# Optimization experiments

Hardware: AMD Instinct MI355X
Metric: run time of the kernel (lower is better)

## Reference

```python
import jax, jax.numpy as jnp
import numpy as np

B, T, D = 2, 2048, 1024
P, ALPHA, P_R = 512, 4, 64
HID = 16 * D
EPS = 1e-6


def rmsnorm(x, w):
    norm = jnp.sqrt(jnp.mean(x * x, axis=-1, keepdims=True) + EPS)
    return x * w / norm


def ssm_lowrank(t, F, b_r, c_r):
    # gated elementwise recurrence h_t = F_t * h_{t-1} + t_t, then low-rank correction
    Fs = jnp.moveaxis(F, 1, 0)   # (T,B,P)
    ts = jnp.moveaxis(t, 1, 0)   # (T,B,P)

    def step(h, inp):
        f, u = inp
        h = f * h + u
        return h, h

    h0 = jnp.zeros((t.shape[0], t.shape[2]), dtype=t.dtype)
    _, hs = jax.lax.scan(step, h0, (Fs, ts))
    h = jnp.moveaxis(hs, 0, 1)   # (B,T,P)
    t_tilde = t + jnp.einsum('btp,pr,rq->btq', h, b_r, c_r)
    return t_tilde


def setup_inputs() -> dict:
    key = jax.random.key(0)
    ks = jax.random.split(key, 11)
    s = lambda fan: 1.0 / np.sqrt(fan)
    return {
        'x':       jax.random.normal(ks[0], (B, T, D), jnp.float32),
        'w_norm1': jnp.ones((D,), jnp.float32),
        'w_toP':   jax.random.normal(ks[1], (D, P), jnp.float32) * s(D),
        'w_emb':   jax.random.normal(ks[2], (D, ALPHA * P), jnp.float32) * s(D),
        'w_f':     jax.random.normal(ks[3], (D, P), jnp.float32) * s(D),
        'b_r':     jax.random.normal(ks[4], (P, P_R), jnp.float32) * s(P),
        'c_r':     jax.random.normal(ks[5], (P_R, P), jnp.float32) * s(P_R),
        'w_fromP': jax.random.normal(ks[6], (P, D), jnp.float32) * s(P),
        'w_norm2': jnp.ones((D,), jnp.float32),
        'w_fc1':   jax.random.normal(ks[7], (D, HID), jnp.float32) * s(D),
        'w_fc2':   jax.random.normal(ks[8], (HID, D), jnp.float32) * s(HID),
    }


def reference(x, w_norm1, w_toP, w_emb, w_f, b_r, c_r, w_fromP, w_norm2, w_fc1, w_fc2):
    # ---- pre-LN CEPTA context path ----
    h1 = rmsnorm(x, w_norm1)
    pre_path = jnp.einsum('btd,dp->btp', h1, w_toP)                 # to_P
    U = jnp.einsum('btd,dk->btk', h1, w_emb).reshape(B, T, ALPHA, P)  # cepta_dense U
    Fgate = jax.nn.sigmoid(jnp.einsum('btd,dp->btp', h1, w_f))      # cepta_dense F
    Y = jax.nn.gelu(U)                                              # cepta_dense Y
    t = jnp.sum(Y, axis=2) + pre_path                               # router reduce='sum'
    t_tilde = ssm_lowrank(t, Fgate, b_r, c_r)                       # low-rank SSM
    y = jnp.einsum('btp,pd->btd', t_tilde, w_fromP)                 # from_P
    x = x + y
    # ---- pre-LN GELU MLP ----
    h2 = rmsnorm(x, w_norm2)
    z = jnp.einsum('bth,hd->btd', jax.nn.gelu(jnp.einsum('btd,dh->bth', h2, w_fc1)), w_fc2)
    return x + z
```

## Files before the change

kernel.cpp:

```cpp
#include <hip/hip_runtime.h>

typedef unsigned short u16;
typedef __bf16 bf16x8 __attribute__((ext_vector_type(8)));
typedef float f32x4 __attribute__((ext_vector_type(4)));
typedef int i32x4 __attribute__((ext_vector_type(4)));

__device__ inline u16 f2bf(float f) {
  union { float f; unsigned u; } v; v.f = f;
  unsigned u = v.u;
  unsigned r = (u + 0x7FFFu + ((u >> 16) & 1u)) >> 16;
  return (u16)r;
}

__device__ inline float gelu_f(float x) {
  float t = 0.7978845608028654f * (x + 0.044715f * x * x * x);
  float a = __expf(-2.f * fabsf(t));
  float th = (1.f - a) / (1.f + a);
  th = copysignf(th, t);
  return 0.5f * x * (1.f + th);
}
__device__ inline float sigmoid_f(float x) { return 1.f / (1.f + __expf(-x)); }

__device__ __forceinline__ void gld16(const u16* g, u16* l) {
  __builtin_amdgcn_global_load_lds((const __attribute__((address_space(1))) void*)g,
                                   (__attribute__((address_space(3))) void*)l, 16, 0, 0);
}
__device__ __forceinline__ bf16x8 ld_frag(const u16* p) {
  return __builtin_bit_cast(bf16x8, *(const i32x4*)p);
}

__global__ void transpose_cvt(const float* __restrict__ in, u16* __restrict__ out,
                              int R, int C, int ldout) {
  __shared__ float tile[32][33];
  int c0 = blockIdx.x * 32, r0 = blockIdx.y * 32;
  int tx = threadIdx.x, ty = threadIdx.y;
#pragma unroll
  for (int i = 0; i < 32; i += 8) {
    int r = r0 + ty + i, c = c0 + tx;
    tile[ty + i][tx] = (r < R && c < C) ? in[(long)r * C + c] : 0.f;
  }
  __syncthreads();
#pragma unroll
  for (int i = 0; i < 32; i += 8) {
    int cc = c0 + ty + i, rr = r0 + tx;
    if (cc < C && rr < R) out[(long)cc * ldout + rr] = f2bf(tile[tx][ty + i]);
  }
}

__global__ __launch_bounds__(256) void rmsnorm_k(const float* __restrict__ x,
                                                 const float* __restrict__ w,
                                                 u16* __restrict__ out) {
  int row = blockIdx.x;
  int tid = threadIdx.x;
  const float4* xv = (const float4*)(x + (long)row * 1024);
  float4 v = xv[tid];
  float ss = v.x * v.x + v.y * v.y + v.z * v.z + v.w * v.w;
#pragma unroll
  for (int off = 32; off > 0; off >>= 1) ss += __shfl_down(ss, off);
  __shared__ float red[4];
  if ((tid & 63) == 0) red[tid >> 6] = ss;
  __syncthreads();
  float tot = red[0] + red[1] + red[2] + red[3];
  float scale = rsqrtf(tot * (1.f / 1024.f) + 1e-6f);
  const float4* wv4 = (const float4*)w;
  float4 wv = wv4[tid];
  ushort4 o;
  o.x = f2bf(v.x * wv.x * scale);
  o.y = f2bf(v.y * wv.y * scale);
  o.z = f2bf(v.z * wv.z * scale);
  o.w = f2bf(v.w * wv.w * scale);
  *((ushort4*)(out + (long)row * 1024) + tid) = o;
}

#define EPI_BF16 0
#define EPI_ROUTE1 1
#define EPI_ADD_BF16 2
#define EPI_ADD_F32 3
#define EPI_GELU_BF16 4
#define EPI_PART 5

template <int EPI>
__global__ __launch_bounds__(512, 2) void gemm256(
    const u16* __restrict__ A, const u16* __restrict__ Bt,
    u16* __restrict__ obf, float* __restrict__ of32,
    float* __restrict__ og, float* __restrict__ ofl,
    int N, int K, int lda, int ldb) {
  __shared__ __align__(16) u16 sA[2][16384];
  __shared__ __align__(16) u16 sB[2][16384];
  const int tid = threadIdx.x;
  const int lane = tid & 63;
  const int wave = tid >> 6;
  const int wm = wave >> 2, wn = wave & 3;
  const int lane15 = lane & 15;

  const int gx = gridDim.x, gy = gridDim.y, gz = gridDim.z;
  const int nwg = gx * gy * gz;
  int orig = (blockIdx.z * gy + blockIdx.y) * gx + blockIdx.x;
  int id = ((nwg & 7) == 0) ? ((orig & 7) * (nwg >> 3) + (orig >> 3)) : orig;
  const int bx = id % gx;
  const int by = (id / gx) % gy;
  const int bz = id / (gx * gy);
  const int bm0 = by * 256, bn0 = bx * 256;
  const int kper = K / gz, koff = bz * kper;

  f32x4 acc[8][4];
  f32x4 zero = {0.f, 0.f, 0.f, 0.f};
#pragma unroll
  for (int m = 0; m < 8; ++m)
#pragma unroll
    for (int n = 0; n < 4; ++n) acc[m][n] = zero;

  const int grow = tid >> 2;
  const int gck = ((tid & 3) ^ ((tid >> 3) & 3)) << 3;
  const u16* ag = A + (long)(bm0 + grow) * lda + koff + gck;
  const u16* bg = Bt + (long)(bn0 + grow) * ldb + koff + gck;
  const long a128 = (long)128 * lda, b128 = (long)128 * ldb;
  const int wofs = wave << 9;

  const int coff = (((lane >> 4) ^ ((lane15 >> 1) & 3)) << 3);
  const int rbrow = (wn & 1) * 64 + lane15;
  const int bsegh = (wn >> 1) * 2;

  const int nk = kper >> 6;

  gld16(ag, &sA[0][0 * 4096 + wofs]);
  gld16(ag + a128, &sA[0][2 * 4096 + wofs]);
  gld16(bg, &sB[0][0 * 4096 + wofs]);
  gld16(bg + b128, &sB[0][2 * 4096 + wofs]);
  gld16(ag + 32, &sA[0][1 * 4096 + wofs]);
  gld16(ag + a128 + 32, &sA[0][3 * 4096 + wofs]);
  gld16(bg + 32, &sB[0][1 * 4096 + wofs]);
  gld16(bg + b128 + 32, &sB[0][3 * 4096 + wofs]);

  bf16x8 av[4], bv[4];
#define DSRD_B(kk)                                                                   \
  _Pragma("unroll") for (int n = 0; n < 4; ++n)                                      \
      bv[n] = ld_frag(rB + (bsegh + kk) * 4096 + (rbrow + n * 16) * 32 + coff);
#define DSRD_A(kk, mh)                                                               \
  _Pragma("unroll") for (int m = 0; m < 4; ++m)                                      \
      av[m] = ld_frag(rA + (wm * 2 + kk) * 4096 + (mh * 64 + m * 16 + lane15) * 32 + coff);
#define MFMA16(mh)                                                                   \
  __builtin_amdgcn_s_setprio(1);                                                     \
  _Pragma("unroll") for (int m = 0; m < 4; ++m)                                      \
      _Pragma("unroll") for (int n = 0; n < 4; ++n)                                  \
          acc[mh * 4 + m][n] =                                                       \
              __builtin_amdgcn_mfma_f32_16x16x32_bf16(av[m], bv[n], acc[mh * 4 + m][n], 0, 0, 0); \
  __builtin_amdgcn_s_setprio(0);
#define WAIT4()                                     \
  asm volatile("s_waitcnt vmcnt(4)" ::: "memory");  \
  __builtin_amdgcn_s_barrier();                     \
  asm volatile("" ::: "memory")
#define WAIT0()                                     \
  asm volatile("s_waitcnt vmcnt(0)" ::: "memory");  \
  __builtin_amdgcn_s_barrier();                     \
  asm volatile("" ::: "memory")

  int p = 0;
  for (int t = 0; t < nk - 1; ++t) {
    const u16* agn = ag + (long)(t + 1) * 64;
    const u16* bgn = bg + (long)(t + 1) * 64;
    u16* dA = &sA[p ^ 1][0];
    u16* dB = &sB[p ^ 1][0];
    const u16* rA = &sA[p][0];
    const u16* rB = &sB[p][0];
    WAIT4();
    DSRD_B(0);
    DSRD_A(0, 0);
    gld16(agn, dA + 0 * 4096 + wofs);
    gld16(agn + a128, dA + 2 * 4096 + wofs);
    MFMA16(0);
    DSRD_A(0, 1);
    gld16(bgn, dB + 0 * 4096 + wofs);
    gld16(bgn + b128, dB + 2 * 4096 + wofs);
    MFMA16(1);
    WAIT4();
    DSRD_B(1);
    DSRD_A(1, 0);
    gld16(agn + 32, dA + 1 * 4096 + wofs);
    gld16(agn + a128 + 32, dA + 3 * 4096 + wofs);
    MFMA16(0);
    DSRD_A(1, 1);
    gld16(bgn + 32, dB + 1 * 4096 + wofs);
    gld16(bgn + b128 + 32, dB + 3 * 4096 + wofs);
    MFMA16(1);
    p ^= 1;
  }
  {
    const u16* rA = &sA[p][0];
    const u16* rB = &sB[p][0];
    WAIT4();
    DSRD_B(0);
    DSRD_A(0, 0);
    MFMA16(0);
    DSRD_A(0, 1);
    MFMA16(1);
    WAIT0();
    DSRD_B(1);
    DSRD_A(1, 0);
    MFMA16(0);
    DSRD_A(1, 1);
    MFMA16(1);
  }
#undef DSRD_B
#undef DSRD_A
#undef MFMA16
#undef WAIT4
#undef WAIT0

#pragma unroll
  for (int M = 0; M < 8; ++M) {
    int row_b = bm0 + wm * 128 + M * 16 + ((lane >> 4) << 2);
#pragma unroll
    for (int n = 0; n < 4; ++n) {
      int col = bn0 + wn * 64 + n * 16 + lane15;
#pragma unroll
      for (int j = 0; j < 4; ++j) {
        int row = row_b + j;
        float v = acc[M][n][j];
        if constexpr (EPI == EPI_GELU_BF16) {
          obf[(long)row * N + col] = f2bf(gelu_f(v));
        } else if constexpr (EPI == EPI_ROUTE1) {
          if (col < 512) of32[(long)row * 512 + col] = v;
          else if (col < 2560) og[(long)row * 2048 + (col - 512)] = gelu_f(v);
          else ofl[(long)row * 512 + (col - 2560)] = sigmoid_f(v);
        } else {
          of32[(long)bz * (4096L * 1024) + (long)row * N + col] = v;
        }
      }
    }
  }
}

template <int EPI>
__global__ __launch_bounds__(256) void gemm_bt(
    const u16* __restrict__ A, const u16* __restrict__ Bt,
    u16* __restrict__ obf, float* __restrict__ of32, const float* __restrict__ add,
    float* __restrict__ og, float* __restrict__ ofl,
    int N, int K, int lda, int ldb) {
  __shared__ __align__(16) u16 As[128 * 64];
  __shared__ __align__(16) u16 Bs[128 * 64];
  const int tid = threadIdx.x;
  const int lane = tid & 63;
  const int wave = tid >> 6;
  const int wm = wave >> 1, wn = wave & 1;
  const int bm0 = blockIdx.y * 128, bn0 = blockIdx.x * 128;

  f32x4 acc[4][4];
  f32x4 zero = {0.f, 0.f, 0.f, 0.f};
#pragma unroll
  for (int m = 0; m < 4; ++m)
#pragma unroll
    for (int n = 0; n < 4; ++n) acc[m][n] = zero;

  i32x4 ra[4], rb[4];
  int srow[4], schk[4];
#pragma unroll
  for (int i = 0; i < 4; ++i) {
    int s = tid + 256 * i;
    srow[i] = s >> 3;
    schk[i] = s & 7;
  }
#pragma unroll
  for (int i = 0; i < 4; ++i) {
    ra[i] = *(const i32x4*)(A + (bm0 + srow[i]) * lda + schk[i] * 8);
    rb[i] = *(const i32x4*)(Bt + (bn0 + srow[i]) * ldb + schk[i] * 8);
  }

  const int nk = K >> 6;
  for (int t = 0; t < nk; ++t) {
#pragma unroll
    for (int i = 0; i < 4; ++i) {
      *(i32x4*)&As[srow[i] * 64 + ((schk[i] ^ (srow[i] & 7)) << 3)] = ra[i];
      *(i32x4*)&Bs[srow[i] * 64 + ((schk[i] ^ (srow[i] & 7)) << 3)] = rb[i];
    }
    __syncthreads();
    if (t + 1 < nk) {
      int k0 = (t + 1) << 6;
#pragma unroll
      for (int i = 0; i < 4; ++i) {
        ra[i] = *(const i32x4*)(A + (bm0 + srow[i]) * lda + k0 + schk[i] * 8);
        rb[i] = *(const i32x4*)(Bt + (bn0 + srow[i]) * ldb + k0 + schk[i] * 8);
      }
    }
#pragma unroll
    for (int kk = 0; kk < 2; ++kk) {
      bf16x8 av[4], bv[4];
#pragma unroll
      for (int m = 0; m < 4; ++m) {
        int r = wm * 64 + m * 16 + (lane & 15);
        int c = kk * 4 + (lane >> 4);
        av[m] = __builtin_bit_cast(bf16x8, *(const i32x4*)&As[r * 64 + ((c ^ (r & 7)) << 3)]);
      }
#pragma unroll
      for (int n = 0; n < 4; ++n) {
        int r = wn * 64 + n * 16 + (lane & 15);
        int c = kk * 4 + (lane >> 4);
        bv[n] = __builtin_bit_cast(bf16x8, *(const i32x4*)&Bs[r * 64 + ((c ^ (r & 7)) << 3)]);
      }
#pragma unroll
      for (int m = 0; m < 4; ++m)
#pragma unroll
        for (int n = 0; n < 4; ++n)
          acc[m][n] = __builtin_amdgcn_mfma_f32_16x16x32_bf16(av[m], bv[n], acc[m][n], 0, 0, 0);
    }
    __syncthreads();
  }

#pragma unroll
  for (int m = 0; m < 4; ++m) {
    int row_b = bm0 + wm * 64 + m * 16 + ((lane >> 4) << 2);
#pragma unroll
    for (int n = 0; n < 4; ++n) {
      int col = bn0 + wn * 64 + n * 16 + (lane & 15);
#pragma unroll
      for (int j = 0; j < 4; ++j) {
        int row = row_b + j;
        float v = acc[m][n][j];
        if constexpr (EPI == EPI_BF16) {
          obf[(long)row * N + col] = f2bf(v);
        } else if constexpr (EPI == EPI_ADD_BF16) {
          long idx = (long)row * N + col;
          obf[idx] = f2bf(add[idx] + v);
        } else if constexpr (EPI == EPI_ADD_F32) {
          long idx = (long)row * N + col;
          of32[idx] = add[idx] + v;
        }
      }
    }
  }
}

__global__ __launch_bounds__(256) void reduce4_k(const float* __restrict__ base,
                                                 const float* __restrict__ p,
                                                 float* __restrict__ o) {
  long i = (long)blockIdx.x * 256 + threadIdx.x;
  const long PL = 4096L * 1024 / 4;
  float4 b = ((const float4*)base)[i];
  float4 q0 = ((const float4*)p)[i];
  float4 q1 = ((const float4*)p)[i + PL];
  float4 q2 = ((const float4*)p)[i + 2 * PL];
  float4 q3 = ((const float4*)p)[i + 3 * PL];
  float4 r;
  r.x = b.x + q0.x + q1.x + q2.x + q3.x;
  r.y = b.y + q0.y + q1.y + q2.y + q3.y;
  r.z = b.z + q0.z + q1.z + q2.z + q3.z;
  r.w = b.w + q0.w + q1.w + q2.w + q3.w;
  ((float4*)o)[i] = r;
}

__global__ __launch_bounds__(256) void router_k(float* __restrict__ tb, const float* __restrict__ G) {
  int i = blockIdx.x * 256 + threadIdx.x;
  int r = i >> 7, pq = i & 127;
  float4 t = ((float4*)tb)[i];
#pragma unroll
  for (int a = 0; a < 4; ++a) {
    float4 g = *((const float4*)(G + (long)r * 2048 + a * 512) + pq);
    t.x += g.x; t.y += g.y; t.z += g.z; t.w += g.w;
  }
  ((float4*)tb)[i] = t;
}

__global__ void scan_chunk(const float* __restrict__ tb, const float* __restrict__ F,
                           float* __restrict__ abuf, float* __restrict__ ubuf) {
  int b = blockIdx.x >> 5, c = blockIdx.x & 31, pidx = threadIdx.x;
  const float* fp = F + ((long)(b * 2048 + c * 64) * 512) + pidx;
  const float* up = tb + ((long)(b * 2048 + c * 64) * 512) + pidx;
  float A = 1.f, U = 0.f;
#pragma unroll 8
  for (int s = 0; s < 64; ++s) {
    float f = fp[(long)s * 512], u = up[(long)s * 512];
    A = f * A;
    U = f * U + u;
  }
  abuf[(b * 32 + c) * 512 + pidx] = A;
  ubuf[(b * 32 + c) * 512 + pidx] = U;
}

__global__ void scan_combine(const float* __restrict__ abuf, const float* __restrict__ ubuf,
                             float* __restrict__ hstart) {
  int b = blockIdx.x, pidx = threadIdx.x;
  float h = 0.f;
  for (int c = 0; c < 32; ++c) {
    hstart[(b * 32 + c) * 512 + pidx] = h;
    h = abuf[(b * 32 + c) * 512 + pidx] * h + ubuf[(b * 32 + c) * 512 + pidx];
  }
}

__global__ void scan_apply(const float* __restrict__ tb, const float* __restrict__ F,
                           const float* __restrict__ hstart, u16* __restrict__ hbf) {
  int b = blockIdx.x >> 5, c = blockIdx.x & 31, pidx = threadIdx.x;
  const float* fp = F + ((long)(b * 2048 + c * 64) * 512) + pidx;
  const float* up = tb + ((long)(b * 2048 + c * 64) * 512) + pidx;
  u16* op = hbf + ((long)(b * 2048 + c * 64) * 512) + pidx;
  float h = hstart[(b * 32 + c) * 512 + pidx];
#pragma unroll 8
  for (int s = 0; s < 64; ++s) {
    float f = fp[(long)s * 512], u = up[(long)s * 512];
    h = f * h + u;
    op[(long)s * 512] = f2bf(h);
  }
}

extern "C" void kernel_launch(void* const* d_in, const int* in_sizes, int n_in,
                              void* d_out, int out_size, void* d_ws, size_t ws_size,
                              hipStream_t stream) {
  const float* x       = (const float*)d_in[0];
  const float* w_norm1 = (const float*)d_in[1];
  const float* w_toP   = (const float*)d_in[2];
  const float* w_emb   = (const float*)d_in[3];
  const float* w_f     = (const float*)d_in[4];
  const float* b_r     = (const float*)d_in[5];
  const float* c_r     = (const float*)d_in[6];
  const float* w_fromP = (const float*)d_in[7];
  const float* w_norm2 = (const float*)d_in[8];
  const float* w_fc1   = (const float*)d_in[9];
  const float* w_fc2   = (const float*)d_in[10];
  float* out = (float*)d_out;

  char* base = (char*)d_ws;
  size_t off = 0;
  auto alloc = [&](size_t bytes) {
    void* r = base + off;
    off += (bytes + 255) & ~(size_t)255;
    return r;
  };
  u16* W1T     = (u16*)alloc((size_t)3072 * 1024 * 2);
  u16* WfromPT = (u16*)alloc((size_t)1024 * 512 * 2);
  u16* Wfc1T   = (u16*)alloc((size_t)16384 * 1024 * 2);
  u16* Wfc2T   = (u16*)alloc((size_t)1024 * 16384 * 2);
  u16* BrT     = (u16*)alloc((size_t)128 * 512 * 2);
  u16* CrT     = (u16*)alloc((size_t)512 * 128 * 2);
  u16* h1      = (u16*)alloc((size_t)4096 * 1024 * 2);
  float* G     = (float*)alloc((size_t)4096 * 2048 * 4);
  float* F     = (float*)alloc((size_t)4096 * 512 * 4);
  float* tb    = (float*)alloc((size_t)4096 * 512 * 4);
  float* abuf  = (float*)alloc((size_t)2 * 32 * 512 * 4);
  float* ubuf  = (float*)alloc((size_t)2 * 32 * 512 * 4);
  float* hstart= (float*)alloc((size_t)2 * 32 * 512 * 4);
  u16* hbf     = (u16*)alloc((size_t)4096 * 512 * 2);
  u16* g1buf   = (u16*)alloc((size_t)4096 * 128 * 2);
  u16* tt      = (u16*)alloc((size_t)4096 * 512 * 2);
  float* xmid  = (float*)alloc((size_t)4096 * 1024 * 4);
  u16* h2      = (u16*)alloc((size_t)4096 * 1024 * 2);
  u16* a3      = (u16*)alloc((size_t)4096 * 8192 * 2);
  float* part  = (float*)h1;
  (void)ws_size; (void)in_sizes; (void)n_in; (void)out_size;

  dim3 tpb(32, 8);
  transpose_cvt<<<dim3(16, 32), tpb, 0, stream>>>(w_toP, W1T, 1024, 512, 1024);
  transpose_cvt<<<dim3(64, 32), tpb, 0, stream>>>(w_emb, W1T + (size_t)512 * 1024, 1024, 2048, 1024);
  transpose_cvt<<<dim3(16, 32), tpb, 0, stream>>>(w_f, W1T + (size_t)2560 * 1024, 1024, 512, 1024);
  transpose_cvt<<<dim3(32, 16), tpb, 0, stream>>>(w_fromP, WfromPT, 512, 1024, 512);
  transpose_cvt<<<dim3(512, 32), tpb, 0, stream>>>(w_fc1, Wfc1T, 1024, 16384, 1024);
  transpose_cvt<<<dim3(32, 512), tpb, 0, stream>>>(w_fc2, Wfc2T, 16384, 1024, 16384);
  hipMemsetAsync(BrT, 0, (size_t)128 * 512 * 2, stream);
  hipMemsetAsync(CrT, 0, (size_t)512 * 128 * 2, stream);
  transpose_cvt<<<dim3(2, 16), tpb, 0, stream>>>(b_r, BrT, 512, 64, 512);
  transpose_cvt<<<dim3(16, 2), tpb, 0, stream>>>(c_r, CrT, 64, 512, 128);

  rmsnorm_k<<<4096, 256, 0, stream>>>(x, w_norm1, h1);

  gemm256<EPI_ROUTE1><<<dim3(12, 16, 1), 512, 0, stream>>>(h1, W1T, nullptr, tb, G, F,
                                                           3072, 1024, 1024, 1024);
  router_k<<<2048, 256, 0, stream>>>(tb, G);

  scan_chunk<<<64, 512, 0, stream>>>(tb, F, abuf, ubuf);
  scan_combine<<<2, 512, 0, stream>>>(abuf, ubuf, hstart);
  scan_apply<<<64, 512, 0, stream>>>(tb, F, hstart, hbf);

  gemm_bt<EPI_BF16><<<dim3(1, 32), 256, 0, stream>>>(hbf, BrT, g1buf, nullptr, nullptr, nullptr, nullptr,
                                                     128, 512, 512, 512);
  gemm_bt<EPI_ADD_BF16><<<dim3(4, 32), 256, 0, stream>>>(g1buf, CrT, tt, nullptr, tb, nullptr, nullptr,
                                                         512, 128, 128, 128);
  gemm_bt<EPI_ADD_F32><<<dim3(8, 32), 256, 0, stream>>>(tt, WfromPT, nullptr, xmid, x, nullptr, nullptr,
                                                        1024, 512, 512, 512);
  rmsnorm_k<<<4096, 256, 0, stream>>>(xmid, w_norm2, h2);

  for (int c = 0; c < 2; ++c) {
    gemm256<EPI_GELU_BF16><<<dim3(32, 16, 1), 512, 0, stream>>>(
        h2, Wfc1T + (size_t)c * 8192 * 1024, a3, nullptr, nullptr, nullptr,
        8192, 1024, 1024, 1024);
    gemm256<EPI_PART><<<dim3(4, 16, 4), 512, 0, stream>>>(
        a3, Wfc2T + (size_t)c * 8192, nullptr, part, nullptr, nullptr,
        1024, 8192, 8192, 16384);
    reduce4_k<<<4096, 256, 0, stream>>>((c == 0 ? xmid : out), part, out);
  }
}
```

Measured before the change: 537.6 us.

## Rewrite small GEMM with async LDS double-buffering and route first projection through it

Replaces the register-staged 128x128 GEMM with a double-buffered version that uses direct global-to-LDS loads, split-K half-tile waits, MFMA priority hints and a workgroup-index swizzle for cache locality. The first fused projection (to_P/emb/F) moves from the 256-tile kernel to this 128-tile kernel with a larger grid to raise occupancy. The low-rank and from_P GEMMs also use it. This adds more LDS per block and depends on the vmcnt-based wait counting being correct.

New measurement: 538.4 us. No clear change (+0.2%).

```diff
diff --git a/kernel.cpp b/kernel.cpp
--- a/kernel.cpp
+++ b/kernel.cpp
@@ -232,18 +232,26 @@
 }
 
 template <int EPI>
-__global__ __launch_bounds__(256) void gemm_bt(
+__global__ __launch_bounds__(256, 2) void gemm128(
     const u16* __restrict__ A, const u16* __restrict__ Bt,
     u16* __restrict__ obf, float* __restrict__ of32, const float* __restrict__ add,
     float* __restrict__ og, float* __restrict__ ofl,
     int N, int K, int lda, int ldb) {
-  __shared__ __align__(16) u16 As[128 * 64];
-  __shared__ __align__(16) u16 Bs[128 * 64];
+  __shared__ __align__(16) u16 sA[2][8192];
+  __shared__ __align__(16) u16 sB[2][8192];
   const int tid = threadIdx.x;
   const int lane = tid & 63;
   const int wave = tid >> 6;
   const int wm = wave >> 1, wn = wave & 1;
-  const int bm0 = blockIdx.y * 128, bn0 = blockIdx.x * 128;
+  const int lane15 = lane & 15;
+
+  const int gx = gridDim.x, gy = gridDim.y;
+  const int nwg = gx * gy;
+  int orig = blockIdx.y * gx + blockIdx.x;
+  int id = ((nwg & 7) == 0) ? ((orig & 7) * (nwg >> 3) + (orig >> 3)) : orig;
+  const int bx = id % gx;
+  const int by = id / gx;
+  const int bm0 = by * 128, bn0 = bx * 128;
 
   f32x4 acc[4][4];
   f32x4 zero = {0.f, 0.f, 0.f, 0.f};
@@ -252,70 +260,96 @@
 #pragma unroll
     for (int n = 0; n < 4; ++n) acc[m][n] = zero;
 
-  i32x4 ra[4], rb[4];
-  int srow[4], schk[4];
-#pragma unroll
-  for (int i = 0; i < 4; ++i) {
-    int s = tid + 256 * i;
-    srow[i] = s >> 3;
-    schk[i] = s & 7;
-  }
-#pragma unroll
-  for (int i = 0; i < 4; ++i) {
-    ra[i] = *(const i32x4*)(A + (bm0 + srow[i]) * lda + schk[i] * 8);
-    rb[i] = *(const i32x4*)(Bt + (bn0 + srow[i]) * ldb + schk[i] * 8);
-  }
+  const int grow = tid >> 2;
+  const int gck = ((tid & 3) ^ ((tid >> 3) & 3)) << 3;
+  const u16* ag = A + (long)(bm0 + grow) * lda + gck;
+  const u16* bg = Bt + (long)(bn0 + grow) * ldb + gck;
+  const long a64 = (long)64 * lda, b64 = (long)64 * ldb;
+  const int wofs = wave << 9;
+
+  const int coff = (((lane >> 4) ^ ((lane15 >> 1) & 3)) << 3);
 
   const int nk = K >> 6;
-  for (int t = 0; t < nk; ++t) {
-#pragma unroll
-    for (int i = 0; i < 4; ++i) {
-      *(i32x4*)&As[srow[i] * 64 + ((schk[i] ^ (srow[i] & 7)) << 3)] = ra[i];
-      *(i32x4*)&Bs[srow[i] * 64 + ((schk[i] ^ (srow[i] & 7)) << 3)] = rb[i];
-    }
-    __syncthreads();
-    if (t + 1 < nk) {
-      int k0 = (t + 1) << 6;
-#pragma unroll
-      for (int i = 0; i < 4; ++i) {
-        ra[i] = *(const i32x4*)(A + (bm0 + srow[i]) * lda + k0 + schk[i] * 8);
-        rb[i] = *(const i32x4*)(Bt + (bn0 + srow[i]) * ldb + k0 + schk[i] * 8);
-      }
-    }
-#pragma unroll
-    for (int kk = 0; kk < 2; ++kk) {
-      bf16x8 av[4], bv[4];
-#pragma unroll
-      for (int m = 0; m < 4; ++m) {
-        int r = wm * 64 + m * 16 + (lane & 15);
-        int c = kk * 4 + (lane >> 4);
-        av[m] = __builtin_bit_cast(bf16x8, *(const i32x4*)&As[r * 64 + ((c ^ (r & 7)) << 3)]);
-      }
-#pragma unroll
-      for (int n = 0; n < 4; ++n) {
-        int r = wn * 64 + n * 16 + (lane & 15);
-        int c = kk * 4 + (lane >> 4);
-        bv[n] = __builtin_bit_cast(bf16x8, *(const i32x4*)&Bs[r * 64 + ((c ^ (r & 7)) << 3)]);
-      }
-#pragma unroll
-      for (int m = 0; m < 4; ++m)
-#pragma unroll
-        for (int n = 0; n < 4; ++n)
-          acc[m][n] = __builtin_amdgcn_mfma_f32_16x16x32_bf16(av[m], bv[n], acc[m][n], 0, 0, 0);
-    }
-    __syncthreads();
-  }
-
-#pragma unroll
-  for (int m = 0; m < 4; ++m) {
-    int row_b = bm0 + wm * 64 + m * 16 + ((lane >> 4) << 2);
+
+  gld16(ag, &sA[0][0 * 4096 + 0 * 2048 + wofs]);
+  gld16(ag + a64, &sA[0][0 * 4096 + 1 * 2048 + wofs]);
+  gld16(bg, &sB[0][0 * 4096 + 0 * 2048 + wofs]);
+  gld16(bg + b64, &sB[0][0 * 4096 + 1 * 2048 + wofs]);
+  gld16(ag + 32, &sA[0][1 * 4096 + 0 * 2048 + wofs]);
+  gld16(ag + a64 + 32, &sA[0][1 * 4096 + 1 * 2048 + wofs]);
+  gld16(bg + 32, &sB[0][1 * 4096 + 0 * 2048 + wofs]);
+  gld16(bg + b64 + 32, &sB[0][1 * 4096 + 1 * 2048 + wofs]);
+
+  bf16x8 av[4], bv[4];
+#define DSRD128(kk)                                                                      \
+  _Pragma("unroll") for (int m = 0; m < 4; ++m)                                          \
+      av[m] = ld_frag(rA + kk * 4096 + (wm * 64 + m * 16 + lane15) * 32 + coff);         \
+  _Pragma("unroll") for (int n = 0; n < 4; ++n)                                          \
+      bv[n] = ld_frag(rB + kk * 4096 + (wn * 64 + n * 16 + lane15) * 32 + coff);
+#define MFMA16x()                                                                        \
+  __builtin_amdgcn_s_setprio(1);                                                         \
+  _Pragma("unroll") for (int m = 0; m < 4; ++m)                                          \
+      _Pragma("unroll") for (int n = 0; n < 4; ++n)                                      \
+          acc[m][n] = __builtin_amdgcn_mfma_f32_16x16x32_bf16(av[m], bv[n], acc[m][n], 0, 0, 0); \
+  __builtin_amdgcn_s_setprio(0);
+#define WAIT4()                                     \
+  asm volatile("s_waitcnt vmcnt(4)" ::: "memory");  \
+  __builtin_amdgcn_s_barrier();                     \
+  asm volatile("" ::: "memory")
+#define WAIT0()                                     \
+  asm volatile("s_waitcnt vmcnt(0)" ::: "memory");  \
+  __builtin_amdgcn_s_barrier();                     \
+  asm volatile("" ::: "memory")
+
+  int p = 0;
+  for (int t = 0; t < nk - 1; ++t) {
+    const u16* agn = ag + (long)(t + 1) * 64;
+    const u16* bgn = bg + (long)(t + 1) * 64;
+    u16* dA = &sA[p ^ 1][0];
+    u16* dB = &sB[p ^ 1][0];
+    const u16* rA = &sA[p][0];
+    const u16* rB = &sB[p][0];
+    WAIT4();
+    DSRD128(0);
+    gld16(agn, dA + 0 * 2048 + wofs);
+    gld16(agn + a64, dA + 1 * 2048 + wofs);
+    gld16(bgn, dB + 0 * 2048 + wofs);
+    gld16(bgn + b64, dB + 1 * 2048 + wofs);
+    MFMA16x();
+    WAIT4();
+    DSRD128(1);
+    gld16(agn + 32, dA + 4096 + 0 * 2048 + wofs);
+    gld16(agn + a64 + 32, dA + 4096 + 1 * 2048 + wofs);
+    gld16(bgn + 32, dB + 4096 + 0 * 2048 + wofs);
+    gld16(bgn + b64 + 32, dB + 4096 + 1 * 2048 + wofs);
+    MFMA16x();
+    p ^= 1;
+  }
+  {
+    const u16* rA = &sA[p][0];
+    const u16* rB = &sB[p][0];
+    WAIT4();
+    DSRD128(0);
+    MFMA16x();
+    WAIT0();
+    DSRD128(1);
+    MFMA16x();
+  }
+#undef DSRD128
+#undef MFMA16x
+#undef WAIT4
+#undef WAIT0
+
+#pragma unroll
+  for (int M = 0; M < 4; ++M) {
+    int row_b = bm0 + wm * 64 + M * 16 + ((lane >> 4) << 2);
 #pragma unroll
     for (int n = 0; n < 4; ++n) {
-      int col = bn0 + wn * 64 + n * 16 + (lane & 15);
+      int col = bn0 + wn * 64 + n * 16 + lane15;
 #pragma unroll
       for (int j = 0; j < 4; ++j) {
         int row = row_b + j;
-        float v = acc[m][n][j];
+        float v = acc[M][n][j];
         if constexpr (EPI == EPI_BF16) {
           obf[(long)row * N + col] = f2bf(v);
         } else if constexpr (EPI == EPI_ADD_BF16) {
@@ -324,6 +358,10 @@
         } else if constexpr (EPI == EPI_ADD_F32) {
           long idx = (long)row * N + col;
           of32[idx] = add[idx] + v;
+        } else if constexpr (EPI == EPI_ROUTE1) {
+          if (col < 512) of32[(long)row * 512 + col] = v;
+          else if (col < 2560) og[(long)row * 2048 + (col - 512)] = gelu_f(v);
+          else ofl[(long)row * 512 + (col - 2560)] = sigmoid_f(v);
         }
       }
     }
@@ -460,19 +498,19 @@
 
   rmsnorm_k<<<4096, 256, 0, stream>>>(x, w_norm1, h1);
 
-  gemm256<EPI_ROUTE1><<<dim3(12, 16, 1), 512, 0, stream>>>(h1, W1T, nullptr, tb, G, F,
-                                                           3072, 1024, 1024, 1024);
+  gemm128<EPI_ROUTE1><<<dim3(24, 32), 256, 0, stream>>>(h1, W1T, nullptr, tb, nullptr, G, F,
+                                                        3072, 1024, 1024, 1024);
   router_k<<<2048, 256, 0, stream>>>(tb, G);
 
   scan_chunk<<<64, 512, 0, stream>>>(tb, F, abuf, ubuf);
   scan_combine<<<2, 512, 0, stream>>>(abuf, ubuf, hstart);
   scan_apply<<<64, 512, 0, stream>>>(tb, F, hstart, hbf);
 
-  gemm_bt<EPI_BF16><<<dim3(1, 32), 256, 0, stream>>>(hbf, BrT, g1buf, nullptr, nullptr, nullptr, nullptr,
+  gemm128<EPI_BF16><<<dim3(1, 32), 256, 0, stream>>>(hbf, BrT, g1buf, nullptr, nullptr, nullptr, nullptr,
                                                      128, 512, 512, 512);
-  gemm_bt<EPI_ADD_BF16><<<dim3(4, 32), 256, 0, stream>>>(g1buf, CrT, tt, nullptr, tb, nullptr, nullptr,
+  gemm128<EPI_ADD_BF16><<<dim3(4, 32), 256, 0, stream>>>(g1buf, CrT, tt, nullptr, tb, nullptr, nullptr,
                                                          512, 128, 128, 128);
-  gemm_bt<EPI_ADD_F32><<<dim3(8, 32), 256, 0, stream>>>(tt, WfromPT, nullptr, xmid, x, nullptr, nullptr,
+  gemm128<EPI_ADD_F32><<<dim3(8, 32), 256, 0, stream>>>(tt, WfromPT, nullptr, xmid, x, nullptr, nullptr,
                                                         1024, 512, 512, 512);
   rmsnorm_k<<<4096, 256, 0, stream>>>(xmid, w_norm2, h2);
 
```
